# Optimization experiments

Measured on AMD Instinct MI355X. Metric: run time of the kernel, lower is better.

Reference implementation:

```python
import jax, jax.numpy as jnp
import numpy as np

B, L, D, H, F = 64, 200, 256, 8, 2
d = D // H  # head dim 32


def setup_inputs() -> dict:
    key = jax.random.key(0)
    ks = jax.random.split(key, 32)
    n = lambda k, s, sc=0.02: jax.random.normal(k, s, jnp.float32) * sc
    inp = {
        'input_tensor': jax.random.normal(ks[0], (B, L, D), jnp.float32),
        'attribute_table': jax.random.normal(ks[1], (F, B, L, D), jnp.float32),
        'position_embedding': jax.random.normal(ks[2], (B, L, D), jnp.float32),
        'attention_mask': jnp.zeros((B, 1, L, L), jnp.float32),
        'Wq': n(ks[3], (D, D)), 'bq': jnp.zeros((D,), jnp.float32),
        'Wk': n(ks[4], (D, D)), 'bk': jnp.zeros((D,), jnp.float32),
        'Wv': n(ks[5], (D, D)), 'bv': jnp.zeros((D,), jnp.float32),
        'Wqp': n(ks[6], (D, D)), 'bqp': jnp.zeros((D,), jnp.float32),
        'Wkp': n(ks[7], (D, D)), 'bkp': jnp.zeros((D,), jnp.float32),
        'Wqa': n(ks[8], (F, D, D)), 'bqa': jnp.zeros((F, D), jnp.float32),
        'Wka': n(ks[9], (F, D, D)), 'bka': jnp.zeros((F, D), jnp.float32),
        'Wg1': n(ks[10], (L, L)), 'bg1': jnp.zeros((L,), jnp.float32),
        'Wg2': n(ks[11], (L, 1)), 'bg2': jnp.zeros((1,), jnp.float32),
        'Wd': n(ks[12], (D, D)), 'bd': jnp.zeros((D,), jnp.float32),
        'ln_g': jnp.ones((D,), jnp.float32), 'ln_b': jnp.zeros((D,), jnp.float32),
    }
    return inp


def _split(x):  # [B,L,D] -> [B,H,L,d]
    b, l, _ = x.shape
    return x.reshape(b, l, H, d).transpose(0, 2, 1, 3)


def reference(input_tensor, attribute_table, position_embedding, attention_mask,
              Wq, bq, Wk, bk, Wv, bv, Wqp, bqp, Wkp, bkp,
              Wqa, bqa, Wka, bka, Wg1, bg1, Wg2, bg2, Wd, bd, ln_g, ln_b):
    q = _split(input_tensor @ Wq + bq)
    k = _split(input_tensor @ Wk + bk)
    v = _split(input_tensor @ Wv + bv)
    qp = _split(position_embedding @ Wqp + bqp)
    kp = _split(position_embedding @ Wkp + bkp)

    item = jnp.einsum('bhqd,bhkd->bhqk', q, k)
    pos = jnp.einsum('bhqd,bhkd->bhqk', qp, kp)

    qa = jnp.einsum('fbld,fde->fble', attribute_table, Wqa) + bqa[:, None, None, :]
    ka = jnp.einsum('fbld,fde->fble', attribute_table, Wka) + bka[:, None, None, :]
    qa = qa.reshape(F, B, L, H, d).transpose(0, 1, 3, 2, 4)  # [F,B,H,L,d]
    ka = ka.reshape(F, B, L, H, d).transpose(0, 1, 3, 2, 4)
    attr = jnp.einsum('fbhqd,fbhkd->fbhqk', qa, ka)  # [F,B,H,L,L]

    # gate fusion: stack streams on axis -2 -> [B,H,L,F+2,L]
    combined = jnp.concatenate(
        [jnp.moveaxis(attr, 0, -2), item[..., None, :], pos[..., None, :]], axis=-2)
    energy = jax.nn.relu(combined @ Wg1 + bg1) @ Wg2 + bg2  # [B,H,L,F+2,1]
    gate_w = jax.nn.softmax(energy[..., 0], axis=-1)        # [B,H,L,F+2]
    scores = jnp.sum(combined * gate_w[..., None], axis=-2)  # [B,H,L,L]

    scores = scores / np.float32(np.sqrt(d)) + attention_mask
    probs = jax.nn.softmax(scores, axis=-1)
    ctx = jnp.einsum('bhqk,bhkd->bhqd', probs, v)
    ctx = ctx.transpose(0, 2, 1, 3).reshape(B, L, D)

    h = ctx @ Wd + bd + input_tensor
    mu = h.mean(-1, keepdims=True)
    var = ((h - mu) ** 2).mean(-1, keepdims=True)
    return (h - mu) * jax.lax.rsqrt(var + 1e-12) * ln_g + ln_b
```

## Files before the change

### kernel.cpp

```cpp
#include <hip/hip_runtime.h>
#include <hip/hip_bf16.h>

typedef __hip_bfloat16 bf16;
typedef __attribute__((ext_vector_type(8))) short s16x8;
typedef __attribute__((ext_vector_type(4))) float f32x4;

#define PB 64
#define PL 200
#define PD 256
#define PH 8
#define PdH 32
#define GK 224
#define GN 208
#define CSTR 232
#define ASTR 264

__device__ __forceinline__ float bfu(unsigned short u) {
    return __uint_as_float(((unsigned)u) << 16);
}

template <typename T> __device__ __forceinline__ float ldf(const T* p);
template <> __device__ __forceinline__ float ldf<float>(const float* p) { return *p; }
template <> __device__ __forceinline__ float ldf<bf16>(const bf16* p) { return __bfloat162float(*p); }
template <typename T> __device__ __forceinline__ void stf(T* p, float v);
template <> __device__ __forceinline__ void stf<float>(float* p, float v) { *p = v; }
template <> __device__ __forceinline__ void stf<bf16>(bf16* p, float v) { *p = __float2bfloat16(v); }

__device__ __forceinline__ void load32_bf16(const bf16* p, float* o) {
    const ushort4* p4 = reinterpret_cast<const ushort4*>(p);
    #pragma unroll
    for (int u = 0; u < 8; ++u) {
        ushort4 x = p4[u];
        o[4 * u + 0] = bfu(x.x); o[4 * u + 1] = bfu(x.y);
        o[4 * u + 2] = bfu(x.z); o[4 * u + 3] = bfu(x.w);
    }
}

__global__ void detect_mode(const unsigned short* lng_raw, int* flag) {
    if (threadIdx.x == 0 && blockIdx.x == 0)
        *flag = (lng_raw[0] == 0x3F80) ? 1 : 0;
}

__global__ void prep_gate(const void* Wg1, const void* bg1, const void* Wg2,
                          bf16* Wg1p, float* bg1f, float* w2f, const int* mode)
{
    const int i = blockIdx.x * 256 + threadIdx.x;
    const bool bm = (*mode != 0);
    if (i < GN * GK) {
        int n = i / GK, k = i % GK;
        float v = 0.f;
        if (n < PL && k < PL)
            v = bm ? __bfloat162float(((const bf16*)Wg1)[(size_t)k * PL + n])
                   : ((const float*)Wg1)[(size_t)k * PL + n];
        Wg1p[i] = __float2bfloat16(v);
    } else if (i < GN * GK + GN) {
        int j = i - GN * GK;
        bg1f[j] = (j < PL) ? (bm ? __bfloat162float(((const bf16*)bg1)[j])
                                 : ((const float*)bg1)[j]) : 0.f;
    } else if (i < GN * GK + 2 * GN) {
        int j = i - GN * GK - GN;
        w2f[j] = (j < PL) ? (bm ? __bfloat162float(((const bf16*)Wg2)[j])
                                : ((const float*)Wg2)[j]) : 0.f;
    }
}

__global__ void prep_w(
    const void* Wq, const void* Wk, const void* Wv,
    const void* Wqp, const void* Wkp, const void* Wqa, const void* Wka,
    const void* bq, const void* bk, const void* bv,
    const void* bqp, const void* bkp, const void* bqa, const void* bka,
    bf16* Wp, float* biasf, const int* mode)
{
    const int i = blockIdx.x * 256 + threadIdx.x;
    const bool bm = (*mode != 0);
    if (i < 9 * 65536) {
        const int wi = i >> 16, r = i & 65535;
        const int n = r >> 8, k = r & 255;
        const void* wp = Wq; size_t off = 0;
        switch (wi) {
            case 1: wp = Wk;  break; case 2: wp = Wv;  break;
            case 3: wp = Wqp; break; case 4: wp = Wkp; break;
            case 5: wp = Wqa; break; case 6: wp = Wka; break;
            case 7: wp = Wqa; off = 65536; break;
            case 8: wp = Wka; off = 65536; break;
            default: break;
        }
        const size_t src = off + (size_t)k * 256 + n;
        float v = bm ? __bfloat162float(((const bf16*)wp)[src])
                     : ((const float*)wp)[src];
        Wp[i] = __float2bfloat16(v);
    } else if (i < 9 * 65536 + 9 * 256) {
        const int j = i - 9 * 65536;
        const int wi = j >> 8, n = j & 255;
        const void* bp = bq; size_t off = 0;
        switch (wi) {
            case 1: bp = bk;  break; case 2: bp = bv;  break;
            case 3: bp = bqp; break; case 4: bp = bkp; break;
            case 5: bp = bqa; break; case 6: bp = bka; break;
            case 7: bp = bqa; off = 256; break;
            case 8: bp = bka; off = 256; break;
            default: break;
        }
        biasf[j] = bm ? __bfloat162float(((const bf16*)bp)[off + n])
                      : ((const float*)bp)[off + n];
    }
}

template <typename T>
__device__ __forceinline__ void stage_a(const T* src, int m0, bf16 (*Alds)[ASTR])
{
    const int t = threadIdx.x;
    for (int i = t; i < 64 * 32; i += 256) {
        const int row = i >> 5, c8 = (i & 31) * 8;
        bf16 tmp[8];
        #pragma unroll
        for (int j = 0; j < 8; ++j)
            tmp[j] = __float2bfloat16(ldf<T>(&src[(size_t)(m0 + row) * 256 + c8 + j]));
        *reinterpret_cast<s16x8*>(&Alds[row][c8]) =
            *reinterpret_cast<const s16x8*>(tmp);
    }
}

__global__ __launch_bounds__(256) void proj_mfma(
    const void* inp, const void* posem, const void* attr,
    const bf16* __restrict__ Wp, const float* __restrict__ biasf,
    bf16* Qh, bf16* Kh, bf16* Vh, bf16* QPh, bf16* KPh,
    bf16* QAh, bf16* KAh, const int* mode)
{
    __shared__ bf16 Alds[64][ASTR];
    const int g = blockIdx.y;
    const int m0 = blockIdx.x * 64;
    const size_t AS = (size_t)PB * PL * PD;

    const void* src = inp; size_t soff = 0;
    if (g == 1) src = posem;
    else if (g == 2) src = attr;
    else if (g == 3) { src = attr; soff = AS; }

    if (*mode) stage_a<bf16>((const bf16*)src + soff, m0, Alds);
    else       stage_a<float>((const float*)src + soff, m0, Alds);
    __syncthreads();

    const int w0 = (g == 0) ? 0 : (g == 1) ? 3 : (g == 2) ? 5 : 7;
    const int nw = (g == 0) ? 3 : 2;

    const int t = threadIdx.x;
    const int w = t >> 6, lane = t & 63;
    const int lrow = lane & 15, lk8 = lane >> 4;

    bf16* dests[9] = { Qh, Kh, Vh, QPh, KPh, QAh, KAh, QAh, KAh };
    const size_t doffs[9] = { 0, 0, 0, 0, 0, 0, 0, AS, AS };

    for (int wi_i = 0; wi_i < nw; ++wi_i) {
        const int wi = w0 + wi_i;
        f32x4 acc[4][4];
        #pragma unroll
        for (int mt = 0; mt < 4; ++mt)
            #pragma unroll
            for (int nt = 0; nt < 4; ++nt) acc[mt][nt] = (f32x4){0.f, 0.f, 0.f, 0.f};

        #pragma unroll
        for (int kt = 0; kt < 8; ++kt) {
            s16x8 a[4], bb[4];
            #pragma unroll
            for (int mt = 0; mt < 4; ++mt)
                a[mt] = *reinterpret_cast<const s16x8*>(
                    &Alds[mt * 16 + lrow][kt * 32 + lk8 * 8]);
            #pragma unroll
            for (int nt = 0; nt < 4; ++nt) {
                const int n = w * 64 + nt * 16 + lrow;
                bb[nt] = *reinterpret_cast<const s16x8*>(
                    &Wp[(size_t)wi * 65536 + (size_t)n * 256 + kt * 32 + lk8 * 8]);
            }
            #pragma unroll
            for (int mt = 0; mt < 4; ++mt)
                #pragma unroll
                for (int nt = 0; nt < 4; ++nt)
                    acc[mt][nt] = __builtin_amdgcn_mfma_f32_16x16x32_bf16(
                        a[mt], bb[nt], acc[mt][nt], 0, 0, 0);
        }

        bf16* dst = dests[wi] + doffs[wi];
        #pragma unroll
        for (int nt = 0; nt < 4; ++nt) {
            const int n = w * 64 + nt * 16 + lrow;
            const float bia = biasf[wi * 256 + n];
            const int h = n >> 5, dc = n & 31;
            #pragma unroll
            for (int mt = 0; mt < 4; ++mt) {
                #pragma unroll
                for (int rg = 0; rg < 4; ++rg) {
                    const int m = m0 + mt * 16 + lk8 * 4 + rg;
                    const int b = m / PL, l = m % PL;
                    dst[(((size_t)b * PH + h) * PL + l) * PdH + dc] =
                        __float2bfloat16(acc[mt][nt][rg] + bia);
                }
            }
        }
    }
}

template <typename T>
__device__ __forceinline__ void fused_body(
    const bf16* Qh, const bf16* Kh, const bf16* Vh,
    const bf16* QPh, const bf16* KPh, const bf16* QAh, const bf16* KAh,
    const T* mask, const T* bg2,
    const bf16* Wg1p, const float* bg1f, const float* w2f,
    bf16* ctx,
    float (*qside)[8][32], bf16 (*c_bf)[CSTR], float (*probs)[200],
    float (*e_part)[32], float (*gw)[8])
{
    const int qt = blockIdx.x, h = blockIdx.y, b = blockIdx.z;
    const int q0 = qt * 8;
    const int t = threadIdx.x;
    const size_t bh = (size_t)b * PH + h;
    const size_t FS = (size_t)PB * PH * PL * PdH;

    const bf16* Qs[4] = { Qh + bh * (PL * PdH), QPh + bh * (PL * PdH),
                          QAh + bh * (PL * PdH), QAh + FS + bh * (PL * PdH) };
    const bf16* Ks[4] = { Kh + bh * (PL * PdH), KPh + bh * (PL * PdH),
                          KAh + bh * (PL * PdH), KAh + FS + bh * (PL * PdH) };

    for (int i = t; i < 4 * 8 * 32; i += 256) {
        int s = i >> 8, rem = i & 255, r = rem >> 5, d0 = rem & 31;
        qside[s][r][d0] = __bfloat162float(Qs[s][(size_t)(q0 + r) * PdH + d0]);
    }
    __syncthreads();

    for (int k = t; k < PL; k += 256) {
        #pragma unroll
        for (int s = 0; s < 4; ++s) {
            float kv[32];
            load32_bf16(Ks[s] + (size_t)k * PdH, kv);
            #pragma unroll
            for (int r = 0; r < 8; ++r) {
                float a = 0.f;
                #pragma unroll
                for (int d0 = 0; d0 < 32; ++d0) a += kv[d0] * qside[s][r][d0];
                c_bf[s * 8 + r][k] = __float2bfloat16(a);
            }
        }
    }
    for (int i = t; i < 32 * (GK - PL); i += 256) {
        int m = i / (GK - PL), k = PL + i % (GK - PL);
        c_bf[m][k] = __float2bfloat16(0.f);
    }
    __syncthreads();

    {
        const int w = t >> 6, lane = t & 63;
        const int lrow = lane & 15;
        const int lk8 = lane >> 4;
        if (lane < 32) e_part[w][lane] = 0.f;
        for (int p = w; p < 26; p += 4) {
            const int mt = p / 13, nt = p % 13;
            f32x4 acc = {0.f, 0.f, 0.f, 0.f};
            #pragma unroll
            for (int kt = 0; kt < 7; ++kt) {
                s16x8 a = *reinterpret_cast<const s16x8*>(
                    &c_bf[mt * 16 + lrow][kt * 32 + lk8 * 8]);
                s16x8 bb = *reinterpret_cast<const s16x8*>(
                    &Wg1p[(size_t)(nt * 16 + lrow) * GK + kt * 32 + lk8 * 8]);
                acc = __builtin_amdgcn_mfma_f32_16x16x32_bf16(a, bb, acc, 0, 0, 0);
            }
            const int n = nt * 16 + lrow;
            const float b1 = bg1f[n];
            const float w2v = w2f[n];
            float part[4];
            #pragma unroll
            for (int rg = 0; rg < 4; ++rg)
                part[rg] = fmaxf(acc[rg] + b1, 0.f) * w2v;
            #pragma unroll
            for (int off = 1; off < 16; off <<= 1)
                #pragma unroll
                for (int rg = 0; rg < 4; ++rg)
                    part[rg] += __shfl_xor(part[rg], off, 64);
            if (lrow == 0) {
                #pragma unroll
                for (int rg = 0; rg < 4; ++rg)
                    e_part[w][mt * 16 + lk8 * 4 + rg] += part[rg];
            }
        }
    }
    __syncthreads();

    if (t < 8) {
        const float bg2v = ldf<T>(&bg2[0]);
        float ev[4];
        #pragma unroll
        for (int s = 0; s < 4; ++s) {
            ev[s] = bg2v;
            #pragma unroll
            for (int w = 0; w < 4; ++w) ev[s] += e_part[w][s * 8 + t];
        }
        float m = ev[0];
        for (int s = 1; s < 4; ++s) m = fmaxf(m, ev[s]);
        float e[4], sum = 0.f;
        for (int s = 0; s < 4; ++s) { e[s] = expf(ev[s] - m); sum += e[s]; }
        float inv = 1.f / sum;
        for (int s = 0; s < 4; ++s) gw[s][t] = e[s] * inv;
    }
    __syncthreads();

    for (int k = t; k < PL; k += 256) {
        #pragma unroll
        for (int r = 0; r < 8; ++r) {
            float sc = 0.f;
            #pragma unroll
            for (int s = 0; s < 4; ++s)
                sc += __bfloat162float(c_bf[s * 8 + r][k]) * gw[s][r];
            sc = sc * 0.17677669529663689f
               + ldf<T>(&mask[((size_t)b * PL + (q0 + r)) * PL + k]);
            probs[r][k] = sc;
        }
    }
    __syncthreads();

    {
        const int lane = t & 63, w = t >> 6;
        for (int rr = 0; rr < 2; ++rr) {
            const int r = w * 2 + rr;
            float v[4];
            float mx = -1e30f;
            #pragma unroll
            for (int ki = 0; ki < 4; ++ki) {
                int k = lane + 64 * ki;
                v[ki] = (k < PL) ? probs[r][k] : -1e30f;
                mx = fmaxf(mx, v[ki]);
            }
            #pragma unroll
            for (int off = 32; off >= 1; off >>= 1) mx = fmaxf(mx, __shfl_xor(mx, off, 64));
            float sum = 0.f;
            #pragma unroll
            for (int ki = 0; ki < 4; ++ki) {
                int k = lane + 64 * ki;
                if (k < PL) { v[ki] = expf(v[ki] - mx); sum += v[ki]; }
            }
            #pragma unroll
            for (int off = 32; off >= 1; off >>= 1) sum += __shfl_xor(sum, off, 64);
            float inv = 1.f / sum;
            #pragma unroll
            for (int ki = 0; ki < 4; ++ki) {
                int k = lane + 64 * ki;
                if (k < PL) probs[r][k] = v[ki] * inv;
            }
        }
    }
    __syncthreads();

    {
        const int r = t >> 5, dc = t & 31;
        const bf16* vp = Vh + bh * (PL * PdH);
        float a = 0.f;
        for (int k = 0; k < PL; ++k)
            a += probs[r][k] * __bfloat162float(vp[(size_t)k * PdH + dc]);
        ctx[((size_t)b * PL + q0 + r) * PD + h * PdH + dc] = __float2bfloat16(a);
    }
}

__global__ __launch_bounds__(256) void fused_attn_kernel(
    const bf16* Qh, const bf16* Kh, const bf16* Vh,
    const bf16* QPh, const bf16* KPh, const bf16* QAh, const bf16* KAh,
    const void* mask, const void* bg2,
    const bf16* Wg1p, const float* bg1f, const float* w2f,
    bf16* ctx, const int* mode)
{
    __shared__ float qside[4][8][32];
    __shared__ bf16 c_bf[32][CSTR];
    __shared__ float probs[8][200];
    __shared__ float e_part[4][32];
    __shared__ float gw[4][8];
    if (*mode)
        fused_body<bf16>(Qh, Kh, Vh, QPh, KPh, QAh, KAh,
                         (const bf16*)mask, (const bf16*)bg2,
                         Wg1p, bg1f, w2f, ctx,
                         qside, c_bf, probs, e_part, gw);
    else
        fused_body<float>(Qh, Kh, Vh, QPh, KPh, QAh, KAh,
                          (const float*)mask, (const float*)bg2,
                          Wg1p, bg1f, w2f, ctx,
                          qside, c_bf, probs, e_part, gw);
}

template <typename T>
__device__ __forceinline__ void outln_body(
    const bf16* ctxp, const T* inp, const T* Wd, const T* bd,
    const T* lng, const T* lnb, T* out,
    float (*xrow)[256], float (*red)[4])
{
    const size_t row0 = (size_t)blockIdx.x * 8;
    const int t = threadIdx.x, lane = t & 63, w = t >> 6;
    for (int i = t; i < 8 * 256; i += 256) {
        int rr = i >> 8, c = i & 255;
        xrow[rr][c] = __bfloat162float(ctxp[(row0 + rr) * 256 + c]);
    }
    __syncthreads();
    float acc[8] = {};
    for (int k = 0; k < 256; ++k) {
        float wv = ldf<T>(&Wd[(size_t)k * 256 + t]);
        #pragma unroll
        for (int rr = 0; rr < 8; ++rr) acc[rr] += xrow[rr][k] * wv;
    }
    const float bdv = ldf<T>(&bd[t]);
    const float gv = ldf<T>(&lng[t]);
    const float bv = ldf<T>(&lnb[t]);
    for (int rr = 0; rr < 8; ++rr) {
        float hv = acc[rr] + bdv + ldf<T>(&inp[(row0 + rr) * 256 + t]);
        float s = hv;
        #pragma unroll
        for (int off = 32; off >= 1; off >>= 1) s += __shfl_xor(s, off, 64);
        if (lane == 0) red[0][w] = s;
        __syncthreads();
        float mu = (red[0][0] + red[0][1] + red[0][2] + red[0][3]) * (1.f / 256.f);
        float dv = hv - mu;
        float s2 = dv * dv;
        #pragma unroll
        for (int off = 32; off >= 1; off >>= 1) s2 += __shfl_xor(s2, off, 64);
        if (lane == 0) red[1][w] = s2;
        __syncthreads();
        float var = (red[1][0] + red[1][1] + red[1][2] + red[1][3]) * (1.f / 256.f);
        stf<T>(&out[(row0 + rr) * 256 + t], dv * rsqrtf(var + 1e-12f) * gv + bv);
        __syncthreads();
    }
}

__global__ __launch_bounds__(256) void out_ln_kernel(
    const bf16* ctxp, const void* inp, const void* Wd, const void* bd,
    const void* lng, const void* lnb, void* out, const int* mode)
{
    __shared__ float xrow[8][256];
    __shared__ float red[2][4];
    if (*mode)
        outln_body<bf16>(ctxp, (const bf16*)inp, (const bf16*)Wd, (const bf16*)bd,
                         (const bf16*)lng, (const bf16*)lnb, (bf16*)out, xrow, red);
    else
        outln_body<float>(ctxp, (const float*)inp, (const float*)Wd, (const float*)bd,
                          (const float*)lng, (const float*)lnb, (float*)out, xrow, red);
}

extern "C" void kernel_launch(void* const* d_in, const int* in_sizes, int n_in,
                              void* d_out, int out_size, void* d_ws, size_t ws_size,
                              hipStream_t stream)
{
    (void)in_sizes; (void)n_in; (void)out_size; (void)ws_size;

    int* flag = (int*)d_ws;
    char* arena = (char*)d_ws + 256;
    const size_t SZ = (size_t)PB * PH * PL * PdH * 2;
    bf16* Qh  = (bf16*)(arena + 0 * SZ);
    bf16* Kh  = (bf16*)(arena + 1 * SZ);
    bf16* Vh  = (bf16*)(arena + 2 * SZ);
    bf16* QPh = (bf16*)(arena + 3 * SZ);
    bf16* KPh = (bf16*)(arena + 4 * SZ);
    bf16* QAh = (bf16*)(arena + 5 * SZ);
    bf16* KAh = (bf16*)(arena + 7 * SZ);
    bf16*  Wp    = (bf16*)(arena + 9 * SZ);
    float* biasf = (float*)(arena + 9 * SZ + (size_t)9 * 65536 * 2);
    bf16*  ctx   = (bf16*)(arena + 9 * SZ);
    bf16*  Wg1p = (bf16*)(arena + 10 * SZ);
    float* bg1f = (float*)(arena + 10 * SZ + (size_t)GN * GK * 2);
    float* w2f  = (float*)(arena + 10 * SZ + (size_t)GN * GK * 2 + 1024);

    detect_mode<<<1, 64, 0, stream>>>((const unsigned short*)d_in[24], flag);
    prep_gate<<<(GN * GK + 2 * GN + 255) / 256, 256, 0, stream>>>(
        d_in[18], d_in[19], d_in[20], Wg1p, bg1f, w2f, flag);
    prep_w<<<(9 * 65536 + 9 * 256 + 255) / 256, 256, 0, stream>>>(
        d_in[4], d_in[6], d_in[8], d_in[10], d_in[12], d_in[14], d_in[16],
        d_in[5], d_in[7], d_in[9], d_in[11], d_in[13], d_in[15], d_in[17],
        Wp, biasf, flag);

    proj_mfma<<<dim3(200, 4), 256, 0, stream>>>(
        d_in[0], d_in[2], d_in[1], Wp, biasf,
        Qh, Kh, Vh, QPh, KPh, QAh, KAh, flag);

    fused_attn_kernel<<<dim3(25, 8, 64), 256, 0, stream>>>(
        Qh, Kh, Vh, QPh, KPh, QAh, KAh,
        d_in[3], d_in[21], Wg1p, bg1f, w2f, ctx, flag);

    out_ln_kernel<<<dim3(1600), 256, 0, stream>>>(
        ctx, d_in[0], d_in[22], d_in[23], d_in[24], d_in[25], d_out, flag);
}
```

Measured before the change: 565.3 us.

## Move attention score, gate and PV products onto MFMA with transposed V

The fused attention kernel now computes the four QK^T streams and the probs·V product with bf16 MFMA instructions instead of scalar FP32 dot loops, and processes 16 query rows per block instead of 8, halving the grid. The projection kernel writes V transposed into a padded [b,h,d,224] layout so PV can use MFMA B-operand loads directly. Intermediate probabilities are stored in bf16 shared memory. This adds rounding of the pre-softmax scores to bf16 and relies on padding and clamping for the partial last query tile.

```diff
diff --git a/kernel.cpp b/kernel.cpp
--- a/kernel.cpp
+++ b/kernel.cpp
@@ -14,9 +14,14 @@
 #define GN 208
 #define CSTR 232
 #define ASTR 264
+#define VTS 224
 
 __device__ __forceinline__ float bfu(unsigned short u) {
     return __uint_as_float(((unsigned)u) << 16);
+}
+__device__ __forceinline__ unsigned short f2bfu(float v) {
+    bf16 t = __float2bfloat16(v);
+    return *reinterpret_cast<unsigned short*>(&t);
 }
 
 template <typename T> __device__ __forceinline__ float ldf(const T* p);
@@ -25,16 +30,6 @@
 template <typename T> __device__ __forceinline__ void stf(T* p, float v);
 template <> __device__ __forceinline__ void stf<float>(float* p, float v) { *p = v; }
 template <> __device__ __forceinline__ void stf<bf16>(bf16* p, float v) { *p = __float2bfloat16(v); }
-
-__device__ __forceinline__ void load32_bf16(const bf16* p, float* o) {
-    const ushort4* p4 = reinterpret_cast<const ushort4*>(p);
-    #pragma unroll
-    for (int u = 0; u < 8; ++u) {
-        ushort4 x = p4[u];
-        o[4 * u + 0] = bfu(x.x); o[4 * u + 1] = bfu(x.y);
-        o[4 * u + 2] = bfu(x.z); o[4 * u + 3] = bfu(x.w);
-    }
-}
 
 __global__ void detect_mode(const unsigned short* lng_raw, int* flag) {
     if (threadIdx.x == 0 && blockIdx.x == 0)
@@ -124,7 +119,7 @@
 __global__ __launch_bounds__(256) void proj_mfma(
     const void* inp, const void* posem, const void* attr,
     const bf16* __restrict__ Wp, const float* __restrict__ biasf,
-    bf16* Qh, bf16* Kh, bf16* Vh, bf16* QPh, bf16* KPh,
+    bf16* Qh, bf16* Kh, bf16* Vt, bf16* QPh, bf16* KPh,
     bf16* QAh, bf16* KAh, const int* mode)
 {
     __shared__ bf16 Alds[64][ASTR];
@@ -148,7 +143,7 @@
     const int w = t >> 6, lane = t & 63;
     const int lrow = lane & 15, lk8 = lane >> 4;
 
-    bf16* dests[9] = { Qh, Kh, Vh, QPh, KPh, QAh, KAh, QAh, KAh };
+    bf16* dests[9] = { Qh, Kh, nullptr, QPh, KPh, QAh, KAh, QAh, KAh };
     const size_t doffs[9] = { 0, 0, 0, 0, 0, 0, 0, AS, AS };
 
     for (int wi_i = 0; wi_i < nw; ++wi_i) {
@@ -180,39 +175,61 @@
                         a[mt], bb[nt], acc[mt][nt], 0, 0, 0);
         }
 
-        bf16* dst = dests[wi] + doffs[wi];
-        #pragma unroll
-        for (int nt = 0; nt < 4; ++nt) {
-            const int n = w * 64 + nt * 16 + lrow;
-            const float bia = biasf[wi * 256 + n];
-            const int h = n >> 5, dc = n & 31;
-            #pragma unroll
-            for (int mt = 0; mt < 4; ++mt) {
+        if (wi == 2) {
+            #pragma unroll
+            for (int nt = 0; nt < 4; ++nt) {
+                const int n = w * 64 + nt * 16 + lrow;
+                const float bia = biasf[wi * 256 + n];
+                const int h = n >> 5, dc = n & 31;
                 #pragma unroll
-                for (int rg = 0; rg < 4; ++rg) {
-                    const int m = m0 + mt * 16 + lk8 * 4 + rg;
-                    const int b = m / PL, l = m % PL;
-                    dst[(((size_t)b * PH + h) * PL + l) * PdH + dc] =
-                        __float2bfloat16(acc[mt][nt][rg] + bia);
+                for (int mt = 0; mt < 4; ++mt) {
+                    const int mq = m0 + mt * 16 + lk8 * 4;
+                    const int b = mq / PL, l0 = mq % PL;
+                    ushort4 pk;
+                    pk.x = f2bfu(acc[mt][nt][0] + bia);
+                    pk.y = f2bfu(acc[mt][nt][1] + bia);
+                    pk.z = f2bfu(acc[mt][nt][2] + bia);
+                    pk.w = f2bfu(acc[mt][nt][3] + bia);
+                    *reinterpret_cast<ushort4*>(
+                        &Vt[(((size_t)b * PH + h) * PdH + dc) * VTS + l0]) = pk;
                 }
             }
+        } else {
+            bf16* dst = dests[wi] + doffs[wi];
+            #pragma unroll
+            for (int nt = 0; nt < 4; ++nt) {
+                const int n = w * 64 + nt * 16 + lrow;
+                const float bia = biasf[wi * 256 + n];
+                const int h = n >> 5, dc = n & 31;
+                #pragma unroll
+                for (int mt = 0; mt < 4; ++mt) {
+                    #pragma unroll
+                    for (int rg = 0; rg < 4; ++rg) {
+                        const int m = m0 + mt * 16 + lk8 * 4 + rg;
+                        const int b = m / PL, l = m % PL;
+                        dst[(((size_t)b * PH + h) * PL + l) * PdH + dc] =
+                            __float2bfloat16(acc[mt][nt][rg] + bia);
+                    }
+                }
+            }
         }
     }
 }
 
 template <typename T>
 __device__ __forceinline__ void fused_body(
-    const bf16* Qh, const bf16* Kh, const bf16* Vh,
+    const bf16* Qh, const bf16* Kh, const bf16* Vt,
     const bf16* QPh, const bf16* KPh, const bf16* QAh, const bf16* KAh,
     const T* mask, const T* bg2,
     const bf16* Wg1p, const float* bg1f, const float* w2f,
     bf16* ctx,
-    float (*qside)[8][32], bf16 (*c_bf)[CSTR], float (*probs)[200],
-    float (*e_part)[32], float (*gw)[8])
+    bf16 (*c_bf)[CSTR], bf16 (*P_bf)[CSTR], float* e_sum, float (*gw)[16])
 {
     const int qt = blockIdx.x, h = blockIdx.y, b = blockIdx.z;
-    const int q0 = qt * 8;
+    const int q0 = qt * 16;
     const int t = threadIdx.x;
+    const int w = t >> 6, lane = t & 63;
+    const int lrow = lane & 15, lk8 = lane >> 4;
     const size_t bh = (size_t)b * PH + h;
     const size_t FS = (size_t)PB * PH * PL * PdH;
 
@@ -221,47 +238,52 @@
     const bf16* Ks[4] = { Kh + bh * (PL * PdH), KPh + bh * (PL * PdH),
                           KAh + bh * (PL * PdH), KAh + FS + bh * (PL * PdH) };
 
-    for (int i = t; i < 4 * 8 * 32; i += 256) {
-        int s = i >> 8, rem = i & 255, r = rem >> 5, d0 = rem & 31;
-        qside[s][r][d0] = __bfloat162float(Qs[s][(size_t)(q0 + r) * PdH + d0]);
-    }
-    __syncthreads();
-
-    for (int k = t; k < PL; k += 256) {
-        #pragma unroll
-        for (int s = 0; s < 4; ++s) {
-            float kv[32];
-            load32_bf16(Ks[s] + (size_t)k * PdH, kv);
-            #pragma unroll
-            for (int r = 0; r < 8; ++r) {
-                float a = 0.f;
+    {
+        const bf16* Qp = Qs[w];
+        const bf16* Kp = Ks[w];
+        const s16x8 bq = *reinterpret_cast<const s16x8*>(
+            &Qp[(size_t)(q0 + lrow) * PdH + lk8 * 8]);
+        const int row = w * 16 + lrow;
+        #pragma unroll
+        for (int nt = 0; nt < 13; ++nt) {
+            const s16x8 a = *reinterpret_cast<const s16x8*>(
+                &Kp[(size_t)(nt * 16 + lrow) * PdH + lk8 * 8]);
+            f32x4 acc = {0.f, 0.f, 0.f, 0.f};
+            acc = __builtin_amdgcn_mfma_f32_16x16x32_bf16(a, bq, acc, 0, 0, 0);
+            const int col = nt * 16 + lk8 * 4;
+            if (nt < 12) {
+                ushort4 pk;
+                pk.x = f2bfu(acc[0]); pk.y = f2bfu(acc[1]);
+                pk.z = f2bfu(acc[2]); pk.w = f2bfu(acc[3]);
+                *reinterpret_cast<ushort4*>(&c_bf[row][col]) = pk;
+            } else {
                 #pragma unroll
-                for (int d0 = 0; d0 < 32; ++d0) a += kv[d0] * qside[s][r][d0];
-                c_bf[s * 8 + r][k] = __float2bfloat16(a);
+                for (int rg = 0; rg < 4; ++rg)
+                    if (col + rg < PL) c_bf[row][col + rg] = __float2bfloat16(acc[rg]);
             }
         }
     }
-    for (int i = t; i < 32 * (GK - PL); i += 256) {
-        int m = i / (GK - PL), k = PL + i % (GK - PL);
-        c_bf[m][k] = __float2bfloat16(0.f);
+    for (int i = t; i < 64 * 24; i += 256) {
+        int r = i / 24, c = PL + i % 24;
+        c_bf[r][c] = __float2bfloat16(0.f);
     }
     __syncthreads();
 
     {
-        const int w = t >> 6, lane = t & 63;
-        const int lrow = lane & 15;
-        const int lk8 = lane >> 4;
-        if (lane < 32) e_part[w][lane] = 0.f;
-        for (int p = w; p < 26; p += 4) {
-            const int mt = p / 13, nt = p % 13;
+        s16x8 a[7];
+        #pragma unroll
+        for (int kt = 0; kt < 7; ++kt)
+            a[kt] = *reinterpret_cast<const s16x8*>(
+                &c_bf[w * 16 + lrow][kt * 32 + lk8 * 8]);
+        float tot[4] = {0.f, 0.f, 0.f, 0.f};
+        #pragma unroll
+        for (int nt = 0; nt < 13; ++nt) {
             f32x4 acc = {0.f, 0.f, 0.f, 0.f};
             #pragma unroll
             for (int kt = 0; kt < 7; ++kt) {
-                s16x8 a = *reinterpret_cast<const s16x8*>(
-                    &c_bf[mt * 16 + lrow][kt * 32 + lk8 * 8]);
-                s16x8 bb = *reinterpret_cast<const s16x8*>(
+                const s16x8 bb = *reinterpret_cast<const s16x8*>(
                     &Wg1p[(size_t)(nt * 16 + lrow) * GK + kt * 32 + lk8 * 8]);
-                acc = __builtin_amdgcn_mfma_f32_16x16x32_bf16(a, bb, acc, 0, 0, 0);
+                acc = __builtin_amdgcn_mfma_f32_16x16x32_bf16(a[kt], bb, acc, 0, 0, 0);
             }
             const int n = nt * 16 + lrow;
             const float b1 = bg1f[n];
@@ -277,22 +299,22 @@
                     part[rg] += __shfl_xor(part[rg], off, 64);
             if (lrow == 0) {
                 #pragma unroll
-                for (int rg = 0; rg < 4; ++rg)
-                    e_part[w][mt * 16 + lk8 * 4 + rg] += part[rg];
+                for (int rg = 0; rg < 4; ++rg) tot[rg] += part[rg];
             }
         }
-    }
-    __syncthreads();
-
-    if (t < 8) {
+        if (lrow == 0) {
+            #pragma unroll
+            for (int rg = 0; rg < 4; ++rg)
+                e_sum[w * 16 + lk8 * 4 + rg] = tot[rg];
+        }
+    }
+    __syncthreads();
+
+    if (t < 16) {
         const float bg2v = ldf<T>(&bg2[0]);
         float ev[4];
         #pragma unroll
-        for (int s = 0; s < 4; ++s) {
-            ev[s] = bg2v;
-            #pragma unroll
-            for (int w = 0; w < 4; ++w) ev[s] += e_part[w][s * 8 + t];
-        }
+        for (int s = 0; s < 4; ++s) ev[s] = bg2v + e_sum[s * 16 + t];
         float m = ev[0];
         for (int s = 1; s < 4; ++s) m = fmaxf(m, ev[s]);
         float e[4], sum = 0.f;
@@ -302,84 +324,91 @@
     }
     __syncthreads();
 
-    for (int k = t; k < PL; k += 256) {
-        #pragma unroll
-        for (int r = 0; r < 8; ++r) {
+    for (int r = 0; r < 16; ++r) {
+        if (t < PL) {
             float sc = 0.f;
             #pragma unroll
             for (int s = 0; s < 4; ++s)
-                sc += __bfloat162float(c_bf[s * 8 + r][k]) * gw[s][r];
+                sc += __bfloat162float(c_bf[s * 16 + r][t]) * gw[s][r];
+            int mr = q0 + r; if (mr > PL - 1) mr = PL - 1;
             sc = sc * 0.17677669529663689f
-               + ldf<T>(&mask[((size_t)b * PL + (q0 + r)) * PL + k]);
-            probs[r][k] = sc;
-        }
-    }
-    __syncthreads();
-
-    {
-        const int lane = t & 63, w = t >> 6;
-        for (int rr = 0; rr < 2; ++rr) {
-            const int r = w * 2 + rr;
-            float v[4];
-            float mx = -1e30f;
-            #pragma unroll
-            for (int ki = 0; ki < 4; ++ki) {
-                int k = lane + 64 * ki;
-                v[ki] = (k < PL) ? probs[r][k] : -1e30f;
-                mx = fmaxf(mx, v[ki]);
-            }
-            #pragma unroll
-            for (int off = 32; off >= 1; off >>= 1) mx = fmaxf(mx, __shfl_xor(mx, off, 64));
-            float sum = 0.f;
-            #pragma unroll
-            for (int ki = 0; ki < 4; ++ki) {
-                int k = lane + 64 * ki;
-                if (k < PL) { v[ki] = expf(v[ki] - mx); sum += v[ki]; }
-            }
-            #pragma unroll
-            for (int off = 32; off >= 1; off >>= 1) sum += __shfl_xor(sum, off, 64);
-            float inv = 1.f / sum;
-            #pragma unroll
-            for (int ki = 0; ki < 4; ++ki) {
-                int k = lane + 64 * ki;
-                if (k < PL) probs[r][k] = v[ki] * inv;
-            }
-        }
-    }
-    __syncthreads();
-
-    {
-        const int r = t >> 5, dc = t & 31;
-        const bf16* vp = Vh + bh * (PL * PdH);
-        float a = 0.f;
-        for (int k = 0; k < PL; ++k)
-            a += probs[r][k] * __bfloat162float(vp[(size_t)k * PdH + dc]);
-        ctx[((size_t)b * PL + q0 + r) * PD + h * PdH + dc] = __float2bfloat16(a);
+               + ldf<T>(&mask[((size_t)b * PL + mr) * PL + t]);
+            P_bf[r][t] = __float2bfloat16(sc);
+        } else if (t < GK) {
+            P_bf[r][t] = __float2bfloat16(0.f);
+        }
+    }
+    __syncthreads();
+
+    for (int rr = 0; rr < 4; ++rr) {
+        const int r = w * 4 + rr;
+        float v[4];
+        float mx = -1e30f;
+        #pragma unroll
+        for (int ki = 0; ki < 4; ++ki) {
+            int k = lane + 64 * ki;
+            v[ki] = (k < PL) ? __bfloat162float(P_bf[r][k]) : -1e30f;
+            mx = fmaxf(mx, v[ki]);
+        }
+        #pragma unroll
+        for (int off = 32; off >= 1; off >>= 1) mx = fmaxf(mx, __shfl_xor(mx, off, 64));
+        float sum = 0.f;
+        #pragma unroll
+        for (int ki = 0; ki < 4; ++ki) {
+            int k = lane + 64 * ki;
+            if (k < PL) { v[ki] = expf(v[ki] - mx); sum += v[ki]; }
+        }
+        #pragma unroll
+        for (int off = 32; off >= 1; off >>= 1) sum += __shfl_xor(sum, off, 64);
+        float inv = 1.f / sum;
+        #pragma unroll
+        for (int ki = 0; ki < 4; ++ki) {
+            int k = lane + 64 * ki;
+            if (k < PL) P_bf[r][k] = __float2bfloat16(v[ki] * inv);
+        }
+    }
+    __syncthreads();
+
+    if (w < 2) {
+        f32x4 acc = {0.f, 0.f, 0.f, 0.f};
+        #pragma unroll
+        for (int kt = 0; kt < 7; ++kt) {
+            const s16x8 a = *reinterpret_cast<const s16x8*>(
+                &P_bf[lrow][kt * 32 + lk8 * 8]);
+            const s16x8 bv = *reinterpret_cast<const s16x8*>(
+                &Vt[((size_t)bh * PdH + w * 16 + lrow) * VTS + kt * 32 + lk8 * 8]);
+            acc = __builtin_amdgcn_mfma_f32_16x16x32_bf16(a, bv, acc, 0, 0, 0);
+        }
+        const int d = w * 16 + lrow;
+        #pragma unroll
+        for (int rg = 0; rg < 4; ++rg) {
+            const int q = q0 + lk8 * 4 + rg;
+            if (q < PL)
+                ctx[((size_t)b * PL + q) * PD + h * PdH + d] =
+                    __float2bfloat16(acc[rg]);
+        }
     }
 }
 
 __global__ __launch_bounds__(256) void fused_attn_kernel(
-    const bf16* Qh, const bf16* Kh, const bf16* Vh,
+    const bf16* Qh, const bf16* Kh, const bf16* Vt,
     const bf16* QPh, const bf16* KPh, const bf16* QAh, const bf16* KAh,
     const void* mask, const void* bg2,
     const bf16* Wg1p, const float* bg1f, const float* w2f,
     bf16* ctx, const int* mode)
 {
-    __shared__ float qside[4][8][32];
-    __shared__ bf16 c_bf[32][CSTR];
-    __shared__ float probs[8][200];
-    __shared__ float e_part[4][32];
-    __shared__ float gw[4][8];
+    __shared__ bf16 c_bf[64][CSTR];
+    __shared__ bf16 P_bf[16][CSTR];
+    __shared__ float e_sum[64];
+    __shared__ float gw[4][16];
     if (*mode)
-        fused_body<bf16>(Qh, Kh, Vh, QPh, KPh, QAh, KAh,
+        fused_body<bf16>(Qh, Kh, Vt, QPh, KPh, QAh, KAh,
                          (const bf16*)mask, (const bf16*)bg2,
-                         Wg1p, bg1f, w2f, ctx,
-                         qside, c_bf, probs, e_part, gw);
+                         Wg1p, bg1f, w2f, ctx, c_bf, P_bf, e_sum, gw);
     else
-        fused_body<float>(Qh, Kh, Vh, QPh, KPh, QAh, KAh,
+        fused_body<float>(Qh, Kh, Vt, QPh, KPh, QAh, KAh,
                           (const float*)mask, (const float*)bg2,
-                          Wg1p, bg1f, w2f, ctx,
-                          qside, c_bf, probs, e_part, gw);
+                          Wg1p, bg1f, w2f, ctx, c_bf, P_bf, e_sum, gw);
 }
 
 template <typename T>
@@ -449,17 +478,17 @@
     const size_t SZ = (size_t)PB * PH * PL * PdH * 2;
     bf16* Qh  = (bf16*)(arena + 0 * SZ);
     bf16* Kh  = (bf16*)(arena + 1 * SZ);
-    bf16* Vh  = (bf16*)(arena + 2 * SZ);
-    bf16* QPh = (bf16*)(arena + 3 * SZ);
-    bf16* KPh = (bf16*)(arena + 4 * SZ);
-    bf16* QAh = (bf16*)(arena + 5 * SZ);
-    bf16* KAh = (bf16*)(arena + 7 * SZ);
-    bf16*  Wp    = (bf16*)(arena + 9 * SZ);
-    float* biasf = (float*)(arena + 9 * SZ + (size_t)9 * 65536 * 2);
-    bf16*  ctx   = (bf16*)(arena + 9 * SZ);
-    bf16*  Wg1p = (bf16*)(arena + 10 * SZ);
-    float* bg1f = (float*)(arena + 10 * SZ + (size_t)GN * GK * 2);
-    float* w2f  = (float*)(arena + 10 * SZ + (size_t)GN * GK * 2 + 1024);
+    bf16* QPh = (bf16*)(arena + 2 * SZ);
+    bf16* KPh = (bf16*)(arena + 3 * SZ);
+    bf16* QAh = (bf16*)(arena + 4 * SZ);
+    bf16* KAh = (bf16*)(arena + 6 * SZ);
+    bf16*  Wp    = (bf16*)(arena + 8 * SZ);
+    float* biasf = (float*)(arena + 8 * SZ + (size_t)9 * 65536 * 2);
+    bf16*  ctx   = (bf16*)(arena + 8 * SZ);
+    bf16*  Wg1p = (bf16*)(arena + 9 * SZ);
+    float* bg1f = (float*)(arena + 9 * SZ + (size_t)GN * GK * 2);
+    float* w2f  = (float*)(arena + 9 * SZ + (size_t)GN * GK * 2 + 1024);
+    bf16*  Vt   = (bf16*)(arena + 9 * SZ + 131072);
 
     detect_mode<<<1, 64, 0, stream>>>((const unsigned short*)d_in[24], flag);
     prep_gate<<<(GN * GK + 2 * GN + 255) / 256, 256, 0, stream>>>(
@@ -471,10 +500,10 @@
 
     proj_mfma<<<dim3(200, 4), 256, 0, stream>>>(
         d_in[0], d_in[2], d_in[1], Wp, biasf,
-        Qh, Kh, Vh, QPh, KPh, QAh, KAh, flag);
-
-    fused_attn_kernel<<<dim3(25, 8, 64), 256, 0, stream>>>(
-        Qh, Kh, Vh, QPh, KPh, QAh, KAh,
+        Qh, Kh, Vt, QPh, KPh, QAh, KAh, flag);
+
+    fused_attn_kernel<<<dim3(13, 8, 64), 256, 0, stream>>>(
+        Qh, Kh, Vt, QPh, KPh, QAh, KAh,
         d_in[3], d_in[21], Wg1p, bg1f, w2f, ctx, flag);
 
     out_ln_kernel<<<dim3(1600), 256, 0, stream>>>(
```

New measurement: 683.9 us. 1.21x slower.
